# Kernel optimization log

Measured on AMD Instinct MI355X. Metric: run time of the kernel, lower is better.

The kernel has to match this reference:

```python
import jax, jax.numpy as jnp
import numpy as np

B, S, H = 32, 256, 128
K, C, DSUB, O = 8, 4096, 16, 6  # PQ subspaces, ncentroids=4096, subvector dim, bits/symbol


def setup_inputs() -> dict:
    key = jax.random.key(0)
    ks = jax.random.split(key, 8)
    return {
        "z": jax.random.normal(ks[0], (B, S, 3), jnp.float32),
        "W1": jax.random.normal(ks[1], (3, H), jnp.float32) * 0.3,
        "b1": jax.random.normal(ks[2], (H,), jnp.float32) * 0.1,
        "W2": jax.random.normal(ks[3], (H, H), jnp.float32) * 0.1,
        "b2": jax.random.normal(ks[4], (H,), jnp.float32) * 0.1,
        "centroids": jax.random.normal(ks[5], (K, C, DSUB), jnp.float32),
        "W3": jax.random.normal(ks[6], (H, O), jnp.float32) * 0.1,
        "b3": jax.random.normal(ks[7], (O,), jnp.float32) * 0.1,
    }


def reference(z, W1, b1, W2, b2, centroids, W3, b3):
    # Small demapper MLP (layers 1-2, exact dense math)
    h1 = jax.nn.relu(z @ W1 + b1)            # [B,S,H]
    h2 = jax.nn.relu(h1 @ W2 + b2)           # [B,S,H] == layer3in
    N = B * S
    x = h2.reshape(N, K, DSUB)               # split rows into K PQ subvectors
    # Encode: nearest centroid per subspace (||x-c||^2 argmin; ||x||^2 is constant per row)
    dots = jnp.einsum("nkd,kcd->nkc", x, centroids)      # [N,K,C]
    c_norm = jnp.sum(centroids * centroids, axis=-1)      # [K,C]
    codes = jnp.argmin(c_norm[None, :, :] - 2.0 * dots, axis=-1)  # [N,K] int
    # LUT: precomputed centroid @ W3 per subspace
    W3r = W3.reshape(K, DSUB, O)
    lut = jnp.einsum("kcd,kdo->kco", centroids, W3r)      # [K,C,O]
    # Approximate matmul: sum of LUT entries selected by codes
    approx = jnp.sum(lut[jnp.arange(K)[None, :], codes], axis=1)  # [N,O]
    llr = (approx + b3).reshape(B, S * O)                 # [B, n]
    return llr
```

## Files before the change

kernel.cpp:

```cpp
#include <hip/hip_runtime.h>
#include <hip/hip_fp16.h>
#include <stdint.h>

#define NROWS 8192
#define HDIM  128
#define KSUB  8
#define NC    4096
#define DSUB  16
#define OUTD  6

#define FB_TAU 6e-5f
#define DOTSCALE (-2.0f / 4096.0f)

typedef _Float16 f16x8 __attribute__((ext_vector_type(8)));
typedef float    f32x4 __attribute__((ext_vector_type(4)));

#define XK_OFF 0u
#define CN_OFF 4194304u
#define B1_OFF 4325376u
#define PK_OFF 6422528u

__global__ __launch_bounds__(256) void prep_kernel(
    const float* __restrict__ z, const float* __restrict__ W1, const float* __restrict__ b1,
    const float* __restrict__ W2, const float* __restrict__ b2,
    const float* __restrict__ ce,
    float* __restrict__ xk, float* __restrict__ cnorm, f16x8* __restrict__ B1S)
{
    __shared__ float h1s[16 * HDIM];
    __shared__ float w2s[HDIM * HDIM];
    const int t = threadIdx.x;
    const int row0 = blockIdx.x * 16;

    {
        const int e = blockIdx.x * 256 + t;
        const int k    = e >> 14;
        const int tile = (e >> 6) & 255;
        const int lane = e & 63;
        const int col  = lane & 15;
        const int quad = lane >> 4;
        const int dims = (quad & 1) * 8;
        const int part = quad >> 1;
        const int n = tile * 16 + col;
        const float* cp = &ce[((size_t)k * NC + n) * DSUB + dims];
        f16x8 hi, lo;
        #pragma unroll
        for (int j = 0; j < 8; ++j) {
            const float s = cp[j] * 16.0f;
            const _Float16 h = (_Float16)s;
            hi[j] = h;
            lo[j] = (_Float16)(s - (float)h);
        }
        B1S[e] = part ? lo : hi;
    }

    if (blockIdx.x < (KSUB * NC) / 256) {
        const int g = blockIdx.x * 256 + t;
        const float4* cp = (const float4*)&ce[(size_t)g * DSUB];
        float nn = 0.f;
        #pragma unroll
        for (int q = 0; q < 4; ++q) {
            const float4 v = cp[q];
            nn = fmaf(v.x, v.x, nn); nn = fmaf(v.y, v.y, nn);
            nn = fmaf(v.z, v.z, nn); nn = fmaf(v.w, v.w, nn);
        }
        cnorm[g] = nn;
    }

    {
        const float4* g4 = (const float4*)W2;
        float4* s4 = (float4*)w2s;
        #pragma unroll
        for (int q = 0; q < 16; ++q) s4[t + q * 256] = g4[t + q * 256];
    }

    #pragma unroll
    for (int e = 0; e < 8; ++e) {
        const int idx = e * 256 + t;
        const int r = idx >> 7, j = idx & 127;
        const int n = row0 + r;
        float acc = b1[j];
        acc = fmaf(z[n * 3 + 0], W1[0 * HDIM + j], acc);
        acc = fmaf(z[n * 3 + 1], W1[1 * HDIM + j], acc);
        acc = fmaf(z[n * 3 + 2], W1[2 * HDIM + j], acc);
        h1s[idx] = fmaxf(acc, 0.f);
    }
    __syncthreads();

    const int c4 = (t & 31) * 4;
    const int r2 = (t >> 5) * 2;
    float acc[2][4];
    #pragma unroll
    for (int a = 0; a < 2; ++a)
        #pragma unroll
        for (int b = 0; b < 4; ++b) acc[a][b] = 0.f;

    for (int k4 = 0; k4 < HDIM; k4 += 4) {
        float hh[2][4], ww[4][4];
        #pragma unroll
        for (int q = 0; q < 2; ++q) {
            const float4 v = *(const float4*)&h1s[(r2 + q) * HDIM + k4];
            hh[q][0] = v.x; hh[q][1] = v.y; hh[q][2] = v.z; hh[q][3] = v.w;
        }
        #pragma unroll
        for (int p = 0; p < 4; ++p) {
            const float4 v = *(const float4*)&w2s[(k4 + p) * HDIM + c4];
            ww[p][0] = v.x; ww[p][1] = v.y; ww[p][2] = v.z; ww[p][3] = v.w;
        }
        #pragma unroll
        for (int q = 0; q < 2; ++q)
            #pragma unroll
            for (int p = 0; p < 4; ++p) {
                acc[q][0] = fmaf(hh[q][p], ww[p][0], acc[q][0]);
                acc[q][1] = fmaf(hh[q][p], ww[p][1], acc[q][1]);
                acc[q][2] = fmaf(hh[q][p], ww[p][2], acc[q][2]);
                acc[q][3] = fmaf(hh[q][p], ww[p][3], acc[q][3]);
            }
    }

    const float4 bb = *(const float4*)&b2[c4];
    const int kk = c4 >> 4;
    const int dd = c4 & 15;
    #pragma unroll
    for (int q = 0; q < 2; ++q) {
        float4 o;
        o.x = fmaxf(acc[q][0] + bb.x, 0.f);
        o.y = fmaxf(acc[q][1] + bb.y, 0.f);
        o.z = fmaxf(acc[q][2] + bb.z, 0.f);
        o.w = fmaxf(acc[q][3] + bb.w, 0.f);
        *(float4*)&xk[((size_t)kk * NROWS + (row0 + r2 + q)) * DSUB + dd] = o;
    }
}

__global__ __launch_bounds__(256, 8) void argmin_kernel(
    const float* __restrict__ xk, const f16x8* __restrict__ B1S,
    const float* __restrict__ cnorm, unsigned long long* __restrict__ pk)
{
    __shared__ f16x8 cs[8 * 64];
    __shared__ float cnL[1024];
    const int t = threadIdx.x;
    const int lane = t & 63;
    const int wid  = t >> 6;
    const int k  = blockIdx.y;
    const int cz = blockIdx.z;
    const int rb = blockIdx.x * 4 + wid;
    const int col  = lane & 15;
    const int quad = lane >> 4;
    const int dims = (quad & 1) * 8;
    const int part = quad >> 1;

    {
        const float* cnp0 = &cnorm[k * NC + cz * 1024];
        #pragma unroll
        for (int q = 0; q < 4; ++q) cnL[t + q * 256] = cnp0[t + q * 256];
    }

    f16x8 A[2];
    #pragma unroll
    for (int g = 0; g < 2; ++g) {
        const int row = rb * 32 + g * 16 + col;
        const float* xp = &xk[((size_t)k * NROWS + row) * DSUB + dims];
        f16x8 hi, lo;
        #pragma unroll
        for (int j = 0; j < 8; ++j) {
            const float s = xp[j] * 256.0f;
            const _Float16 h = (_Float16)s;
            hi[j] = h;
            lo[j] = (_Float16)(s - (float)h);
        }
        A[g] = part ? lo : hi;
    }

    float m1[2][4], m2[2][4];
    int   idx[2][4];
    #pragma unroll
    for (int g = 0; g < 2; ++g)
        #pragma unroll
        for (int j = 0; j < 4; ++j) { m1[g][j] = 1e30f; m2[g][j] = 1e30f; idx[g][j] = 0; }

    const f16x8* gp = &B1S[((size_t)k * 256 + cz * 64) * 64];

    for (int ch = 0; ch < 8; ++ch) {
        __syncthreads();
        {
            const uint4* g4 = (const uint4*)(gp + (size_t)ch * 512);
            uint4* s4 = (uint4*)cs;
            #pragma unroll
            for (int q = 0; q < 2; ++q) s4[t + q * 256] = g4[t + q * 256];
        }
        __syncthreads();

        #pragma unroll 2
        for (int tt = 0; tt < 8; ++tt) {
            const f16x8 b1 = cs[tt * 64 + lane];
            const f16x8 b2 = cs[tt * 64 + (lane ^ 32)];
            const float nrm = cnL[(ch * 8 + tt) * 16 + col];
            const f32x4 zz = {0.f, 0.f, 0.f, 0.f};
            f32x4 p0 = __builtin_amdgcn_mfma_f32_16x16x32_f16(A[0], b1, zz, 0, 0, 0);
            p0       = __builtin_amdgcn_mfma_f32_16x16x32_f16(A[0], b2, p0, 0, 0, 0);
            f32x4 p1 = __builtin_amdgcn_mfma_f32_16x16x32_f16(A[1], b1, zz, 0, 0, 0);
            p1       = __builtin_amdgcn_mfma_f32_16x16x32_f16(A[1], b2, p1, 0, 0, 0);
            const int c = ((cz * 64 + ch * 8 + tt) << 4) + col;
            #pragma unroll
            for (int j = 0; j < 4; ++j) {
                {
                    const float s = fmaf(p0[j], DOTSCALE, nrm);
                    const bool lt = s < m1[0][j];
                    m2[0][j] = __builtin_amdgcn_fmed3f(s, m1[0][j], m2[0][j]);
                    idx[0][j] = lt ? c : idx[0][j];
                    m1[0][j] = fminf(s, m1[0][j]);
                }
                {
                    const float s = fmaf(p1[j], DOTSCALE, nrm);
                    const bool lt = s < m1[1][j];
                    m2[1][j] = __builtin_amdgcn_fmed3f(s, m1[1][j], m2[1][j]);
                    idx[1][j] = lt ? c : idx[1][j];
                    m1[1][j] = fminf(s, m1[1][j]);
                }
            }
        }
    }

    #pragma unroll
    for (int off = 1; off < 16; off <<= 1) {
        #pragma unroll
        for (int g = 0; g < 2; ++g)
            #pragma unroll
            for (int j = 0; j < 4; ++j) {
                const float om1 = __shfl_xor(m1[g][j], off, 64);
                const float om2 = __shfl_xor(m2[g][j], off, 64);
                const int  oidx = __shfl_xor(idx[g][j], off, 64);
                const bool better = (om1 < m1[g][j]) ||
                                    (om1 == m1[g][j] && oidx < idx[g][j]);
                m2[g][j] = fminf(fminf(m2[g][j], om2), fmaxf(m1[g][j], om1));
                m1[g][j] = better ? om1 : m1[g][j];
                idx[g][j] = better ? oidx : idx[g][j];
            }
    }

    if (col == 0) {
        #pragma unroll
        for (int g = 0; g < 2; ++g)
            #pragma unroll
            for (int j = 0; j < 4; ++j) {
                const int row = rb * 32 + g * 16 + quad * 4 + j;
                unsigned u = __float_as_uint(m1[g][j]);
                u = (u & 0x80000000u) ? ~u : (u | 0x80000000u);
                const unsigned short dh =
                    __half_as_ushort(__float2half(m2[g][j] - m1[g][j]));
                pk[((size_t)cz * NROWS + row) * KSUB + k] =
                    ((unsigned long long)u << 32) |
                    ((unsigned)dh << 16) | (unsigned)idx[g][j];
            }
    }
}

__global__ __launch_bounds__(256) void finish_kernel(
    const float* __restrict__ xk, const float* __restrict__ ce,
    const float* __restrict__ cnorm, const unsigned long long* __restrict__ pk,
    const float* __restrict__ W3, const float* __restrict__ b3,
    float* __restrict__ out)
{
    __shared__ int codes_s[256];
    __shared__ int wl_s[256];
    __shared__ int wcnt;
    const int t = threadIdx.x;
    const int row0 = blockIdx.x * 32;
    if (t == 0) wcnt = 0;
    __syncthreads();

    {
        const int row = row0 + (t >> 3);
        const int k = t & 7;
        unsigned long long p[4];
        #pragma unroll
        for (int s = 0; s < 4; ++s)
            p[s] = pk[((size_t)s * NROWS + row) * KSUB + k];
        unsigned long long w = p[0];
        #pragma unroll
        for (int s = 1; s < 4; ++s) w = p[s] < w ? p[s] : w;
        const unsigned uw = (unsigned)(w >> 32);
        const float m1w = __uint_as_float((uw & 0x80000000u) ? (uw ^ 0x80000000u) : ~uw);
        float m2g = m1w + (float)__ushort_as_half((unsigned short)((unsigned)w >> 16));
        #pragma unroll
        for (int s = 0; s < 4; ++s) {
            if (p[s] != w) {
                const unsigned us = (unsigned)(p[s] >> 32);
                m2g = fminf(m2g, __uint_as_float(
                    (us & 0x80000000u) ? (us ^ 0x80000000u) : ~us));
            }
        }
        codes_s[t] = (int)(w & 0xFFFFull);
        if (m2g - m1w < FB_TAU) {
            const int slot = atomicAdd(&wcnt, 1);
            wl_s[slot] = t;
        }
    }
    __syncthreads();

    {
        const int lane = t & 63;
        const int wid = t >> 6;
        const int nitems = wcnt;
        for (int i = wid; i < nitems; i += 4) {
            const int wg = wl_s[i];
            const int row = row0 + (wg >> 3), k = wg & 7;
            float xr[DSUB];
            {
                const float* xp = &xk[((size_t)k * NROWS + row) * DSUB];
                #pragma unroll
                for (int q = 0; q < DSUB; q += 4) {
                    const float4 v = *(const float4*)&xp[q];
                    xr[q + 0] = -2.f * v.x; xr[q + 1] = -2.f * v.y;
                    xr[q + 2] = -2.f * v.z; xr[q + 3] = -2.f * v.w;
                }
            }
            float bm = 1e30f; int bi = NC;
            for (int c = lane; c < NC; c += 64) {
                const float* cp = &ce[((size_t)k * NC + c) * DSUB];
                float s = cnorm[k * NC + c];
                #pragma unroll
                for (int d = 0; d < DSUB; ++d) s = fmaf(xr[d], cp[d], s);
                if (s < bm) { bm = s; bi = c; }
            }
            #pragma unroll
            for (int off = 1; off < 64; off <<= 1) {
                const float om = __shfl_xor(bm, off, 64);
                const int  oi = __shfl_xor(bi, off, 64);
                const bool better = (om < bm) || (om == bm && oi < bi);
                bm = better ? om : bm;
                bi = better ? oi : bi;
            }
            if (lane == 0) codes_s[wg] = bi;
        }
    }
    __syncthreads();

    if (t < 32 * OUTD) {
        const int nl = t / OUTD;
        const int o = t - nl * OUTD;
        const int n = row0 + nl;
        float acc = b3[o];
        #pragma unroll
        for (int k = 0; k < KSUB; ++k) {
            const int code = codes_s[nl * KSUB + k];
            const float* cp = &ce[((size_t)k * NC + code) * DSUB];
            const float* wp = &W3[(k * DSUB) * OUTD + o];
            #pragma unroll
            for (int d = 0; d < DSUB; ++d)
                acc = fmaf(cp[d], wp[d * OUTD], acc);
        }
        out[n * OUTD + o] = acc;
    }
}

extern "C" void kernel_launch(void* const* d_in, const int* in_sizes, int n_in,
                              void* d_out, int out_size, void* d_ws, size_t ws_size,
                              hipStream_t stream)
{
    const float* z  = (const float*)d_in[0];
    const float* W1 = (const float*)d_in[1];
    const float* b1 = (const float*)d_in[2];
    const float* W2 = (const float*)d_in[3];
    const float* b2 = (const float*)d_in[4];
    const float* ce = (const float*)d_in[5];
    const float* W3 = (const float*)d_in[6];
    const float* b3 = (const float*)d_in[7];

    char* ws = (char*)d_ws;
    float* xk    = (float*)(ws + XK_OFF);
    float* cnorm = (float*)(ws + CN_OFF);
    f16x8* B1S   = (f16x8*)(ws + B1_OFF);
    unsigned long long* pk = (unsigned long long*)(ws + PK_OFF);

    hipLaunchKernelGGL(prep_kernel, dim3(512), dim3(256), 0, stream,
                       z, W1, b1, W2, b2, ce, xk, cnorm, B1S);
    hipLaunchKernelGGL(argmin_kernel, dim3(64, 8, 4), dim3(256), 0, stream,
                       xk, B1S, cnorm, pk);
    hipLaunchKernelGGL(finish_kernel, dim3(256), dim3(256), 0, stream,
                       xk, ce, cnorm, pk, W3, b3, (float*)d_out);
}
```

Baseline: 169.9 us.

## Double rows per wave, stream centroids from global, fold norms into MFMA accumulator

```diff
diff --git a/kernel.cpp b/kernel.cpp
--- a/kernel.cpp
+++ b/kernel.cpp
@@ -9,8 +9,9 @@
 #define DSUB  16
 #define OUTD  6
 
-#define FB_TAU 6e-5f
+#define FB_TAU 1.2e-4f
 #define DOTSCALE (-2.0f / 4096.0f)
+#define QSCALE   (-2048.0f)
 
 typedef _Float16 f16x8 __attribute__((ext_vector_type(8)));
 typedef float    f32x4 __attribute__((ext_vector_type(4)));
@@ -131,33 +132,33 @@
     }
 }
 
-__global__ __launch_bounds__(256, 8) void argmin_kernel(
+__global__ __launch_bounds__(256, 4) void argmin_kernel(
     const float* __restrict__ xk, const f16x8* __restrict__ B1S,
     const float* __restrict__ cnorm, unsigned long long* __restrict__ pk)
 {
-    __shared__ f16x8 cs[8 * 64];
     __shared__ float cnL[1024];
     const int t = threadIdx.x;
     const int lane = t & 63;
     const int wid  = t >> 6;
     const int k  = blockIdx.y;
     const int cz = blockIdx.z;
-    const int rb = blockIdx.x * 4 + wid;
     const int col  = lane & 15;
     const int quad = lane >> 4;
     const int dims = (quad & 1) * 8;
     const int part = quad >> 1;
+    const int lane2 = lane ^ 32;
+    const int rowbase = (blockIdx.x * 4 + wid) * 64;
 
     {
         const float* cnp0 = &cnorm[k * NC + cz * 1024];
         #pragma unroll
-        for (int q = 0; q < 4; ++q) cnL[t + q * 256] = cnp0[t + q * 256];
-    }
-
-    f16x8 A[2];
-    #pragma unroll
-    for (int g = 0; g < 2; ++g) {
-        const int row = rb * 32 + g * 16 + col;
+        for (int q = 0; q < 4; ++q) cnL[t + q * 256] = cnp0[t + q * 256] * QSCALE;
+    }
+
+    f16x8 A[4];
+    #pragma unroll
+    for (int g = 0; g < 4; ++g) {
+        const int row = rowbase + g * 16 + col;
         const float* xp = &xk[((size_t)k * NROWS + row) * DSUB + dims];
         f16x8 hi, lo;
         #pragma unroll
@@ -170,68 +171,58 @@
         A[g] = part ? lo : hi;
     }
 
-    float m1[2][4], m2[2][4];
-    int   idx[2][4];
-    #pragma unroll
-    for (int g = 0; g < 2; ++g)
-        #pragma unroll
-        for (int j = 0; j < 4; ++j) { m1[g][j] = 1e30f; m2[g][j] = 1e30f; idx[g][j] = 0; }
+    float m1[4][4], m2[4][4];
+    int   idx[4][4];
+    #pragma unroll
+    for (int g = 0; g < 4; ++g)
+        #pragma unroll
+        for (int j = 0; j < 4; ++j) { m1[g][j] = -1e30f; m2[g][j] = -1e30f; idx[g][j] = 0; }
 
     const f16x8* gp = &B1S[((size_t)k * 256 + cz * 64) * 64];
 
-    for (int ch = 0; ch < 8; ++ch) {
-        __syncthreads();
-        {
-            const uint4* g4 = (const uint4*)(gp + (size_t)ch * 512);
-            uint4* s4 = (uint4*)cs;
-            #pragma unroll
-            for (int q = 0; q < 2; ++q) s4[t + q * 256] = g4[t + q * 256];
-        }
-        __syncthreads();
-
-        #pragma unroll 2
-        for (int tt = 0; tt < 8; ++tt) {
-            const f16x8 b1 = cs[tt * 64 + lane];
-            const f16x8 b2 = cs[tt * 64 + (lane ^ 32)];
-            const float nrm = cnL[(ch * 8 + tt) * 16 + col];
-            const f32x4 zz = {0.f, 0.f, 0.f, 0.f};
-            f32x4 p0 = __builtin_amdgcn_mfma_f32_16x16x32_f16(A[0], b1, zz, 0, 0, 0);
-            p0       = __builtin_amdgcn_mfma_f32_16x16x32_f16(A[0], b2, p0, 0, 0, 0);
-            f32x4 p1 = __builtin_amdgcn_mfma_f32_16x16x32_f16(A[1], b1, zz, 0, 0, 0);
-            p1       = __builtin_amdgcn_mfma_f32_16x16x32_f16(A[1], b2, p1, 0, 0, 0);
-            const int c = ((cz * 64 + ch * 8 + tt) << 4) + col;
+    f16x8 b1 = gp[lane];
+    f16x8 b2 = gp[lane2];
+
+    __syncthreads();
+
+    for (int t64 = 0; t64 < 64; ++t64) {
+        const int nt = (t64 + 1) & 63;
+        f16x8 nb1 = gp[nt * 64 + lane];
+        f16x8 nb2 = gp[nt * 64 + lane2];
+
+        const float nrm = cnL[t64 * 16 + col];
+        const f32x4 ci = {nrm, nrm, nrm, nrm};
+        const int c = ((cz * 64 + t64) << 4) + col;
+
+        #pragma unroll
+        for (int g = 0; g < 4; ++g) {
+            f32x4 p = __builtin_amdgcn_mfma_f32_16x16x32_f16(A[g], b1, ci, 0, 0, 0);
+            p       = __builtin_amdgcn_mfma_f32_16x16x32_f16(A[g], b2, p, 0, 0, 0);
             #pragma unroll
             for (int j = 0; j < 4; ++j) {
-                {
-                    const float s = fmaf(p0[j], DOTSCALE, nrm);
-                    const bool lt = s < m1[0][j];
-                    m2[0][j] = __builtin_amdgcn_fmed3f(s, m1[0][j], m2[0][j]);
-                    idx[0][j] = lt ? c : idx[0][j];
-                    m1[0][j] = fminf(s, m1[0][j]);
-                }
-                {
-                    const float s = fmaf(p1[j], DOTSCALE, nrm);
-                    const bool lt = s < m1[1][j];
-                    m2[1][j] = __builtin_amdgcn_fmed3f(s, m1[1][j], m2[1][j]);
-                    idx[1][j] = lt ? c : idx[1][j];
-                    m1[1][j] = fminf(s, m1[1][j]);
-                }
-            }
-        }
+                const float q = p[j];
+                const bool gt = q > m1[g][j];
+                m2[g][j] = __builtin_amdgcn_fmed3f(q, m1[g][j], m2[g][j]);
+                idx[g][j] = gt ? c : idx[g][j];
+                m1[g][j] = fmaxf(q, m1[g][j]);
+            }
+        }
+        b1 = nb1;
+        b2 = nb2;
     }
 
     #pragma unroll
     for (int off = 1; off < 16; off <<= 1) {
         #pragma unroll
-        for (int g = 0; g < 2; ++g)
+        for (int g = 0; g < 4; ++g)
             #pragma unroll
             for (int j = 0; j < 4; ++j) {
                 const float om1 = __shfl_xor(m1[g][j], off, 64);
                 const float om2 = __shfl_xor(m2[g][j], off, 64);
                 const int  oidx = __shfl_xor(idx[g][j], off, 64);
-                const bool better = (om1 < m1[g][j]) ||
+                const bool better = (om1 > m1[g][j]) ||
                                     (om1 == m1[g][j] && oidx < idx[g][j]);
-                m2[g][j] = fminf(fminf(m2[g][j], om2), fmaxf(m1[g][j], om1));
+                m2[g][j] = fmaxf(fminf(m1[g][j], om1), fmaxf(m2[g][j], om2));
                 m1[g][j] = better ? om1 : m1[g][j];
                 idx[g][j] = better ? oidx : idx[g][j];
             }
@@ -239,14 +230,15 @@
 
     if (col == 0) {
         #pragma unroll
-        for (int g = 0; g < 2; ++g)
+        for (int g = 0; g < 4; ++g)
             #pragma unroll
             for (int j = 0; j < 4; ++j) {
-                const int row = rb * 32 + g * 16 + quad * 4 + j;
-                unsigned u = __float_as_uint(m1[g][j]);
+                const int row = rowbase + g * 16 + quad * 4 + j;
+                const float s1 = m1[g][j] * DOTSCALE;
+                const float dl = (m1[g][j] - m2[g][j]) * (2.0f / 4096.0f);
+                unsigned u = __float_as_uint(s1);
                 u = (u & 0x80000000u) ? ~u : (u | 0x80000000u);
-                const unsigned short dh =
-                    __half_as_ushort(__float2half(m2[g][j] - m1[g][j]));
+                const unsigned short dh = __half_as_ushort(__float2half(dl));
                 pk[((size_t)cz * NROWS + row) * KSUB + k] =
                     ((unsigned long long)u << 32) |
                     ((unsigned)dh << 16) | (unsigned)idx[g][j];
@@ -374,7 +366,7 @@
 
     hipLaunchKernelGGL(prep_kernel, dim3(512), dim3(256), 0, stream,
                        z, W1, b1, W2, b2, ce, xk, cnorm, B1S);
-    hipLaunchKernelGGL(argmin_kernel, dim3(64, 8, 4), dim3(256), 0, stream,
+    hipLaunchKernelGGL(argmin_kernel, dim3(32, 8, 4), dim3(256), 0, stream,
                        xk, B1S, cnorm, pk);
     hipLaunchKernelGGL(finish_kernel, dim3(256), dim3(256), 0, stream,
                        xk, ce, cnorm, pk, W3, b3, (float*)d_out);
```

New measurement: 177.2 us. 1.04x slower.

## Drop centroid split in argmin, widen row tile, prefetch centroid chunks

Applied to the files above, without the earlier changes.

```diff
diff --git a/kernel.cpp b/kernel.cpp
--- a/kernel.cpp
+++ b/kernel.cpp
@@ -131,17 +131,16 @@
     }
 }
 
-__global__ __launch_bounds__(256, 8) void argmin_kernel(
+__global__ __launch_bounds__(256, 4) void argmin_kernel(
     const float* __restrict__ xk, const f16x8* __restrict__ B1S,
-    const float* __restrict__ cnorm, unsigned long long* __restrict__ pk)
+    const float* __restrict__ cnorm, unsigned* __restrict__ pk)
 {
     __shared__ f16x8 cs[8 * 64];
-    __shared__ float cnL[1024];
+    __shared__ float cnL[NC];
     const int t = threadIdx.x;
     const int lane = t & 63;
     const int wid  = t >> 6;
     const int k  = blockIdx.y;
-    const int cz = blockIdx.z;
     const int rb = blockIdx.x * 4 + wid;
     const int col  = lane & 15;
     const int quad = lane >> 4;
@@ -149,15 +148,15 @@
     const int part = quad >> 1;
 
     {
-        const float* cnp0 = &cnorm[k * NC + cz * 1024];
-        #pragma unroll
-        for (int q = 0; q < 4; ++q) cnL[t + q * 256] = cnp0[t + q * 256];
-    }
-
-    f16x8 A[2];
-    #pragma unroll
-    for (int g = 0; g < 2; ++g) {
-        const int row = rb * 32 + g * 16 + col;
+        const float* cnp0 = &cnorm[k * NC];
+        #pragma unroll
+        for (int q = 0; q < 16; ++q) cnL[t + q * 256] = cnp0[t + q * 256];
+    }
+
+    f16x8 A[4];
+    #pragma unroll
+    for (int g = 0; g < 4; ++g) {
+        const int row = rb * 64 + g * 16 + col;
         const float* xp = &xk[((size_t)k * NROWS + row) * DSUB + dims];
         f16x8 hi, lo;
         #pragma unroll
@@ -170,24 +169,35 @@
         A[g] = part ? lo : hi;
     }
 
-    float m1[2][4], m2[2][4];
-    int   idx[2][4];
-    #pragma unroll
-    for (int g = 0; g < 2; ++g)
+    float m1[4][4], m2[4][4];
+    int   idx[4][4];
+    #pragma unroll
+    for (int g = 0; g < 4; ++g)
         #pragma unroll
         for (int j = 0; j < 4; ++j) { m1[g][j] = 1e30f; m2[g][j] = 1e30f; idx[g][j] = 0; }
 
-    const f16x8* gp = &B1S[((size_t)k * 256 + cz * 64) * 64];
-
-    for (int ch = 0; ch < 8; ++ch) {
+    const f16x8* gp = &B1S[(size_t)k * 256 * 64];
+
+    uint4 pre0, pre1;
+    {
+        const uint4* g4 = (const uint4*)gp;
+        pre0 = g4[t];
+        pre1 = g4[t + 256];
+    }
+
+    for (int ch = 0; ch < 32; ++ch) {
         __syncthreads();
         {
-            const uint4* g4 = (const uint4*)(gp + (size_t)ch * 512);
             uint4* s4 = (uint4*)cs;
-            #pragma unroll
-            for (int q = 0; q < 2; ++q) s4[t + q * 256] = g4[t + q * 256];
+            s4[t] = pre0;
+            s4[t + 256] = pre1;
         }
         __syncthreads();
+        if (ch < 31) {
+            const uint4* g4 = (const uint4*)(gp + (size_t)(ch + 1) * 512);
+            pre0 = g4[t];
+            pre1 = g4[t + 256];
+        }
 
         #pragma unroll 2
         for (int tt = 0; tt < 8; ++tt) {
@@ -195,27 +205,19 @@
             const f16x8 b2 = cs[tt * 64 + (lane ^ 32)];
             const float nrm = cnL[(ch * 8 + tt) * 16 + col];
             const f32x4 zz = {0.f, 0.f, 0.f, 0.f};
-            f32x4 p0 = __builtin_amdgcn_mfma_f32_16x16x32_f16(A[0], b1, zz, 0, 0, 0);
-            p0       = __builtin_amdgcn_mfma_f32_16x16x32_f16(A[0], b2, p0, 0, 0, 0);
-            f32x4 p1 = __builtin_amdgcn_mfma_f32_16x16x32_f16(A[1], b1, zz, 0, 0, 0);
-            p1       = __builtin_amdgcn_mfma_f32_16x16x32_f16(A[1], b2, p1, 0, 0, 0);
-            const int c = ((cz * 64 + ch * 8 + tt) << 4) + col;
-            #pragma unroll
-            for (int j = 0; j < 4; ++j) {
-                {
-                    const float s = fmaf(p0[j], DOTSCALE, nrm);
-                    const bool lt = s < m1[0][j];
-                    m2[0][j] = __builtin_amdgcn_fmed3f(s, m1[0][j], m2[0][j]);
-                    idx[0][j] = lt ? c : idx[0][j];
-                    m1[0][j] = fminf(s, m1[0][j]);
+            const int c = ((ch * 8 + tt) << 4) + col;
+            #pragma unroll
+            for (int g = 0; g < 4; ++g) {
+                f32x4 p = __builtin_amdgcn_mfma_f32_16x16x32_f16(A[g], b1, zz, 0, 0, 0);
+                p       = __builtin_amdgcn_mfma_f32_16x16x32_f16(A[g], b2, p, 0, 0, 0);
+                #pragma unroll
+                for (int j = 0; j < 4; ++j) {
+                    const float s = fmaf(p[j], DOTSCALE, nrm);
+                    const bool lt = s < m1[g][j];
+                    m2[g][j] = __builtin_amdgcn_fmed3f(s, m1[g][j], m2[g][j]);
+                    idx[g][j] = lt ? c : idx[g][j];
+                    m1[g][j] = fminf(s, m1[g][j]);
                 }
-                {
-                    const float s = fmaf(p1[j], DOTSCALE, nrm);
-                    const bool lt = s < m1[1][j];
-                    m2[1][j] = __builtin_amdgcn_fmed3f(s, m1[1][j], m2[1][j]);
-                    idx[1][j] = lt ? c : idx[1][j];
-                    m1[1][j] = fminf(s, m1[1][j]);
-                }
             }
         }
     }
@@ -223,7 +225,7 @@
     #pragma unroll
     for (int off = 1; off < 16; off <<= 1) {
         #pragma unroll
-        for (int g = 0; g < 2; ++g)
+        for (int g = 0; g < 4; ++g)
             #pragma unroll
             for (int j = 0; j < 4; ++j) {
                 const float om1 = __shfl_xor(m1[g][j], off, 64);
@@ -239,16 +241,13 @@
 
     if (col == 0) {
         #pragma unroll
-        for (int g = 0; g < 2; ++g)
+        for (int g = 0; g < 4; ++g)
             #pragma unroll
             for (int j = 0; j < 4; ++j) {
-                const int row = rb * 32 + g * 16 + quad * 4 + j;
-                unsigned u = __float_as_uint(m1[g][j]);
-                u = (u & 0x80000000u) ? ~u : (u | 0x80000000u);
+                const int row = rb * 64 + g * 16 + quad * 4 + j;
                 const unsigned short dh =
                     __half_as_ushort(__float2half(m2[g][j] - m1[g][j]));
-                pk[((size_t)cz * NROWS + row) * KSUB + k] =
-                    ((unsigned long long)u << 32) |
+                pk[(size_t)row * KSUB + k] =
                     ((unsigned)dh << 16) | (unsigned)idx[g][j];
             }
     }
@@ -256,7 +255,7 @@
 
 __global__ __launch_bounds__(256) void finish_kernel(
     const float* __restrict__ xk, const float* __restrict__ ce,
-    const float* __restrict__ cnorm, const unsigned long long* __restrict__ pk,
+    const float* __restrict__ cnorm, const unsigned* __restrict__ pk,
     const float* __restrict__ W3, const float* __restrict__ b3,
     float* __restrict__ out)
 {
@@ -271,26 +270,10 @@
     {
         const int row = row0 + (t >> 3);
         const int k = t & 7;
-        unsigned long long p[4];
-        #pragma unroll
-        for (int s = 0; s < 4; ++s)
-            p[s] = pk[((size_t)s * NROWS + row) * KSUB + k];
-        unsigned long long w = p[0];
-        #pragma unroll
-        for (int s = 1; s < 4; ++s) w = p[s] < w ? p[s] : w;
-        const unsigned uw = (unsigned)(w >> 32);
-        const float m1w = __uint_as_float((uw & 0x80000000u) ? (uw ^ 0x80000000u) : ~uw);
-        float m2g = m1w + (float)__ushort_as_half((unsigned short)((unsigned)w >> 16));
-        #pragma unroll
-        for (int s = 0; s < 4; ++s) {
-            if (p[s] != w) {
-                const unsigned us = (unsigned)(p[s] >> 32);
-                m2g = fminf(m2g, __uint_as_float(
-                    (us & 0x80000000u) ? (us ^ 0x80000000u) : ~us));
-            }
-        }
-        codes_s[t] = (int)(w & 0xFFFFull);
-        if (m2g - m1w < FB_TAU) {
+        const unsigned w = pk[(size_t)row * KSUB + k];
+        codes_s[t] = (int)(w & 0xFFFFu);
+        const float gap = (float)__ushort_as_half((unsigned short)(w >> 16));
+        if (gap < FB_TAU) {
             const int slot = atomicAdd(&wcnt, 1);
             wl_s[slot] = t;
         }
@@ -370,11 +353,11 @@
     float* xk    = (float*)(ws + XK_OFF);
     float* cnorm = (float*)(ws + CN_OFF);
     f16x8* B1S   = (f16x8*)(ws + B1_OFF);
-    unsigned long long* pk = (unsigned long long*)(ws + PK_OFF);
+    unsigned* pk = (unsigned*)(ws + PK_OFF);
 
     hipLaunchKernelGGL(prep_kernel, dim3(512), dim3(256), 0, stream,
                        z, W1, b1, W2, b2, ce, xk, cnorm, B1S);
-    hipLaunchKernelGGL(argmin_kernel, dim3(64, 8, 4), dim3(256), 0, stream,
+    hipLaunchKernelGGL(argmin_kernel, dim3(32, 8), dim3(256), 0, stream,
                        xk, B1S, cnorm, pk);
     hipLaunchKernelGGL(finish_kernel, dim3(256), dim3(256), 0, stream,
                        xk, ce, cnorm, pk, W3, b3, (float*)d_out);
```

Measured after the change: 184.5 us. 8.5% more time.
